# Kernel optimization log

Hardware: AMD Instinct MI355X
Metric: run time of the kernel (lower is better)

The kernel has to match this reference:

```python
import jax, jax.numpy as jnp
import numpy as np

N_NODES = 100000
N_EDGES = 1600000
F_IN = 128
HID = 128  # nhid*2
NHID = 64
N_GRAPHS = 512
N_CLASSES = 10
NEG_SLOPE = 0.2  # PyG GATConv default


def setup_inputs() -> dict:
    key = jax.random.key(0)
    ks = jax.random.split(key, 16)
    x = jax.random.normal(ks[0], (N_NODES, F_IN), dtype=jnp.float32)
    edge_index = jax.random.randint(ks[1], (2, N_EDGES), 0, N_NODES, dtype=jnp.int64)
    batch = jnp.sort(jax.random.randint(ks[2], (N_NODES,), 0, N_GRAPHS, dtype=jnp.int64))
    def lin(k, fan_in, shape):
        bound = 1.0 / np.sqrt(fan_in)
        return jax.random.uniform(k, shape, jnp.float32, -bound, bound)
    return {
        "x": x, "edge_index": edge_index, "batch": batch,
        "W1": lin(ks[3], F_IN, (F_IN, HID)),
        "a_src1": lin(ks[4], HID, (HID,)),
        "a_dst1": lin(ks[5], HID, (HID,)),
        "b1": jnp.zeros((HID,), jnp.float32),
        "W2": lin(ks[6], HID, (HID, HID)),
        "a_src2": lin(ks[7], HID, (HID,)),
        "a_dst2": lin(ks[8], HID, (HID,)),
        "b2": jnp.zeros((HID,), jnp.float32),
        "W_fc1": lin(ks[9], HID, (HID, NHID)),
        "b_fc1": lin(ks[10], HID, (NHID,)),
        "W_fc2": lin(ks[11], NHID, (NHID, N_CLASSES)),
        "b_fc2": lin(ks[12], NHID, (N_CLASSES,)),
    }


def gat_conv(x, src, dst, W, a_src, a_dst, b):
    # h = W x ; attention e_ij = LeakyReLU(a_src.h_i + a_dst.h_j), softmax over
    # incoming edges of each destination j, then scatter-add aggregation.
    h = x @ W                                   # [N, H]
    alpha_s = h @ a_src                         # [N]
    alpha_d = h @ a_dst                         # [N]
    e = jax.nn.leaky_relu(alpha_s[src] + alpha_d[dst], NEG_SLOPE)  # [E]
    n = x.shape[0]
    m = jax.ops.segment_max(e, dst, num_segments=n)                # per-dst max
    ex = jnp.exp(e - m[dst])
    denom = jax.ops.segment_sum(ex, dst, num_segments=n)
    alpha = ex / denom[dst]                                        # [E]
    out = jax.ops.segment_sum(alpha[:, None] * h[src], dst, num_segments=n)
    return out + b


def reference(x, edge_index, batch, W1, a_src1, a_dst1, b1,
              W2, a_src2, a_dst2, b2, W_fc1, b_fc1, W_fc2, b_fc2):
    n = x.shape[0]
    # GATConv default add_self_loops=True
    loops = jnp.arange(n, dtype=edge_index.dtype)
    src = jnp.concatenate([edge_index[0], loops])
    dst = jnp.concatenate([edge_index[1], loops])

    h = jax.nn.selu(gat_conv(x, src, dst, W1, a_src1, a_dst1, b1))
    h = jax.nn.selu(gat_conv(h, src, dst, W2, a_src2, a_dst2, b2))

    # global mean pool over graphs
    sums = jax.ops.segment_sum(h, batch, num_segments=N_GRAPHS)
    cnts = jax.ops.segment_sum(jnp.ones((n,), h.dtype), batch, num_segments=N_GRAPHS)
    pooled = jax.nn.selu(sums / jnp.maximum(cnts, 1.0)[:, None])   # [G, H]

    g = jax.nn.selu(pooled @ W_fc1 + b_fc1)
    # dropout p=0.5 is identity in eval mode
    logits = g @ W_fc2 + b_fc2
    return jax.nn.log_softmax(logits, axis=-1)
```

## Files before the change

kernel.cpp:

```cpp
#include <hip/hip_runtime.h>
#include <hip/hip_bf16.h>

#define NEG_SLOPE 0.2f
typedef unsigned int uint32;

#define BSHIFT 9
#define BSIZE 512
#define MAXB 256
#define PCHUNK 4096
#define BSTRIDE 12288

typedef __attribute__((ext_vector_type(8))) __bf16 bf16x8;
typedef __attribute__((ext_vector_type(4))) float f32x4;

__device__ __forceinline__ float selu_f(float x) {
    const float a = 1.6732632423543772f, s = 1.0507009873554805f;
    return x > 0.0f ? s * x : s * a * (__expf(x) - 1.0f);
}

__device__ __forceinline__ unsigned short f2bf(float x) {
    uint32 u = __float_as_uint(x);
    uint32 r = (u + 0x7fff + ((u >> 16) & 1)) >> 16;
    return (unsigned short)r;
}
__device__ __forceinline__ float bf_lo(uint32 g) { return __uint_as_float(g << 16); }
__device__ __forceinline__ float bf_hi(uint32 g) { return __uint_as_float(g & 0xffff0000u); }

__global__ __launch_bounds__(256) void prep9(const float* __restrict__ W1,
                                             const float* __restrict__ W2,
                                             unsigned short* __restrict__ Wb,
                                             const int* __restrict__ batch,
                                             int* __restrict__ gstart,
                                             int N, int G) {
    int b = blockIdx.x, t = threadIdx.x;
    if (b < 2) {
        const float* W = b ? W2 : W1;
        unsigned short* oh = Wb + (size_t)b * 32768;
        unsigned short* ol = oh + 16384;
        for (int d = t; d < 16384; d += 256) {
            int j = d & 7, nn = (d >> 3) & 127, g = d >> 10;
            float v = W[(g * 8 + j) * 128 + nn];
            uint32 hu = f2bf(v);
            float hv = __uint_as_float(hu << 16);
            oh[d] = (unsigned short)hu;
            ol[d] = f2bf(v - hv);
        }
    } else {
        int i = (b - 2) * 256 + t;
        if (i < N) {
            int bb = batch[i];
            int bp = (i == 0) ? -1 : batch[i - 1];
            for (int q = bp + 1; q <= bb; ++q) gstart[q] = i;
            if (i == N - 1)
                for (int q = bb + 1; q <= G; ++q) gstart[q] = N;
        }
    }
}

__global__ __launch_bounds__(256) void partition_edges(const int* __restrict__ ei,
                                                       int* __restrict__ gcur0,
                                                       uint32* __restrict__ tmp,
                                                       int E, int TOT) {
    __shared__ int lcnt[MAXB];
    __shared__ int lstart[MAXB];
    __shared__ int lcur[MAXB];
    __shared__ int gbase[MAXB];
    __shared__ uint32 staged[PCHUNK];
    __shared__ unsigned char bslot[PCHUNK];
    int t = threadIdx.x;
    int eb = blockIdx.x * PCHUNK;
    int sreg[16], dreg[16];
    #pragma unroll
    for (int k = 0; k < 16; ++k) {
        int e = eb + k * 256 + t;
        if (e < TOT) {
            if (e < E) { sreg[k] = ei[e]; dreg[k] = ei[E + e]; }
            else       { sreg[k] = dreg[k] = e - E; }
        } else dreg[k] = -1;
    }
    lcnt[t] = 0;
    __syncthreads();
    #pragma unroll
    for (int k = 0; k < 16; ++k)
        if (dreg[k] >= 0) atomicAdd(&lcnt[dreg[k] >> BSHIFT], 1);
    __syncthreads();
    int v = lcnt[t];
    lstart[t] = v;
    __syncthreads();
    for (int off = 1; off < 256; off <<= 1) {
        int add = (t >= off) ? lstart[t - off] : 0;
        __syncthreads();
        lstart[t] += add;
        __syncthreads();
    }
    int ex = lstart[t] - v;
    __syncthreads();
    lstart[t] = ex;
    lcur[t] = ex;
    if (v > 0) gbase[t] = t * BSTRIDE + atomicAdd(&gcur0[t], v);
    __syncthreads();
    #pragma unroll
    for (int k = 0; k < 16; ++k) {
        int d = dreg[k];
        if (d >= 0) {
            int b = d >> BSHIFT;
            int p = atomicAdd(&lcur[b], 1);
            staged[p] = ((uint32)(d & (BSIZE - 1)) << 17) | (uint32)sreg[k];
            bslot[p] = (unsigned char)b;
        }
    }
    __syncthreads();
    int nvalid = TOT - eb; if (nvalid > PCHUNK) nvalid = PCHUNK;
    for (int i = t; i < nvalid; i += 256) {
        int b = bslot[i];
        tmp[gbase[b] + (i - lstart[b])] = staged[i];
    }
}

__global__ __launch_bounds__(256) void bucket_build(const uint32* __restrict__ tmp,
                                                    const int* __restrict__ gcur0,
                                                    int* __restrict__ rowptr,
                                                    int* __restrict__ rowend,
                                                    int* __restrict__ col,
                                                    int N, int NB) {
    __shared__ int cnt[BSIZE];
    __shared__ int sums[256];
    int b = blockIdx.x, t = threadIdx.x;
    int lo = b << BSHIFT;
    int nn = N - lo; if (nn > BSIZE) nn = BSIZE;
    cnt[t] = 0; cnt[t + 256] = 0;
    __syncthreads();
    int ebeg = b * BSTRIDE;
    int eend = ebeg + gcur0[b];
    for (int i = ebeg + t; i < eend; i += 256)
        atomicAdd(&cnt[tmp[i] >> 17], 1);
    __syncthreads();
    int c0 = cnt[2 * t], c1 = cnt[2 * t + 1];
    int s2 = c0 + c1;
    sums[t] = s2;
    __syncthreads();
    for (int off = 1; off < 256; off <<= 1) {
        int add = (t >= off) ? sums[t - off] : 0;
        __syncthreads();
        sums[t] += add;
        __syncthreads();
    }
    int ex = sums[t] - s2;
    int st0 = ebeg + ex, st1 = st0 + c0;
    if (2 * t < nn)     { rowptr[lo + 2 * t] = st0;     rowend[lo + 2 * t] = st0 + c0; }
    if (2 * t + 1 < nn) { rowptr[lo + 2 * t + 1] = st1; rowend[lo + 2 * t + 1] = st1 + c1; }
    cnt[2 * t] = st0; cnt[2 * t + 1] = st1;
    __syncthreads();
    for (int i = ebeg + t; i < eend; i += 256) {
        uint32 u = tmp[i];
        int p = atomicAdd(&cnt[u >> 17], 1);
        col[p] = (int)(u & 0x1FFFFu);
    }
}

__device__ __forceinline__ void gemm_core(const bf16x8 ah[2][4],
                                          const __bf16* Wl,
                                          const float* a_src, const float* a_dst,
                                          uint32* hb, float* as_, float* ad_,
                                          int rbase, int n, int col16, int quad) {
    f32x4 acc[2][8];
    #pragma unroll
    for (int mt = 0; mt < 2; ++mt)
        #pragma unroll
        for (int t = 0; t < 8; ++t) acc[mt][t] = (f32x4)(0.0f);

    #pragma unroll
    for (int c = 0; c < 4; ++c) {
        #pragma unroll
        for (int t = 0; t < 8; ++t) {
            int off = (((c * 4 + quad) * 128) + t * 16 + col16) * 8;
            bf16x8 bh = *(const bf16x8*)&Wl[off];
            bf16x8 bl = *(const bf16x8*)&Wl[16384 + off];
            #pragma unroll
            for (int mt = 0; mt < 2; ++mt) {
                acc[mt][t] = __builtin_amdgcn_mfma_f32_16x16x32_bf16(ah[mt][c], bh, acc[mt][t], 0, 0, 0);
                acc[mt][t] = __builtin_amdgcn_mfma_f32_16x16x32_bf16(ah[mt][c], bl, acc[mt][t], 0, 0, 0);
            }
        }
    }
    float asv[8], adv[8];
    #pragma unroll
    for (int t = 0; t < 8; ++t) { asv[t] = a_src[t * 16 + col16]; adv[t] = a_dst[t * 16 + col16]; }
    #pragma unroll
    for (int mt = 0; mt < 2; ++mt) {
        #pragma unroll
        for (int reg = 0; reg < 4; ++reg) {
            float s = 0.0f, d = 0.0f;
            #pragma unroll
            for (int t = 0; t < 8; ++t) {
                float v = acc[mt][t][reg];
                s += v * asv[t]; d += v * adv[t];
            }
            #pragma unroll
            for (int off = 1; off < 16; off <<= 1) {
                s += __shfl_xor(s, off);
                d += __shfl_xor(d, off);
            }
            int r = rbase + mt * 16 + quad * 4 + reg;
            if (col16 == 0 && r < n) { as_[r] = s; ad_[r] = d; }
        }
    }
    #pragma unroll
    for (int mt = 0; mt < 2; ++mt)
    #pragma unroll
    for (int t = 0; t < 8; ++t)
    #pragma unroll
    for (int reg = 0; reg < 4; ++reg) {
        float v = acc[mt][t][reg];
        float p = __shfl_xor(v, 1);
        int r = rbase + mt * 16 + quad * 4 + reg;
        if (!(col16 & 1) && r < n) {
            uint32 pk = (uint32)f2bf(v) | ((uint32)f2bf(p) << 16);
            hb[(size_t)r * 64 + t * 8 + (col16 >> 1)] = pk;
        }
    }
}

__global__ __launch_bounds__(256) void gemm_mfma_f32(const float* __restrict__ X,
                                                     const unsigned short* __restrict__ Wbh,
                                                     const float* __restrict__ a_src,
                                                     const float* __restrict__ a_dst,
                                                     uint32* __restrict__ hb,
                                                     float* __restrict__ as_,
                                                     float* __restrict__ ad_, int n) {
    __shared__ __bf16 Wl[32768];
    const int tid = threadIdx.x;
    {
        const uint4* sw = (const uint4*)Wbh;
        uint4* dw = (uint4*)Wl;
        for (int i = tid; i < 4096; i += 256) dw[i] = sw[i];
    }
    const int lane = tid & 63, wid = tid >> 6;
    const int col16 = lane & 15, quad = lane >> 4;
    const int rbase = blockIdx.x * 128 + wid * 32;
    bf16x8 ah[2][4];
    #pragma unroll
    for (int mt = 0; mt < 2; ++mt) {
        int r = rbase + mt * 16 + col16;
        bool ok = (r < n);
        const float* xp = X + (size_t)r * 128;
        #pragma unroll
        for (int c = 0; c < 4; ++c) {
            int k0 = c * 32 + quad * 8;
            float4 x0 = ok ? *(const float4*)(xp + k0)     : make_float4(0.f,0.f,0.f,0.f);
            float4 x1 = ok ? *(const float4*)(xp + k0 + 4) : make_float4(0.f,0.f,0.f,0.f);
            float xs[8] = {x0.x,x0.y,x0.z,x0.w,x1.x,x1.y,x1.z,x1.w};
            #pragma unroll
            for (int j = 0; j < 8; ++j) ah[mt][c][j] = (__bf16)xs[j];
        }
    }
    __syncthreads();
    gemm_core(ah, Wl, a_src, a_dst, hb, as_, ad_, rbase, n, col16, quad);
}

__global__ __launch_bounds__(256) void gemm_mfma_bf16(const __bf16* __restrict__ X,
                                                      const unsigned short* __restrict__ Wbh,
                                                      const float* __restrict__ a_src,
                                                      const float* __restrict__ a_dst,
                                                      uint32* __restrict__ hb,
                                                      float* __restrict__ as_,
                                                      float* __restrict__ ad_, int n) {
    __shared__ __bf16 Wl[32768];
    const int tid = threadIdx.x;
    {
        const uint4* sw = (const uint4*)Wbh;
        uint4* dw = (uint4*)Wl;
        for (int i = tid; i < 4096; i += 256) dw[i] = sw[i];
    }
    const int lane = tid & 63, wid = tid >> 6;
    const int col16 = lane & 15, quad = lane >> 4;
    const int rbase = blockIdx.x * 128 + wid * 32;
    bf16x8 ah[2][4];
    const bf16x8 zz = (bf16x8)((__bf16)0.0f);
    #pragma unroll
    for (int mt = 0; mt < 2; ++mt) {
        int r = rbase + mt * 16 + col16;
        bool ok = (r < n);
        const __bf16* xp = X + (size_t)r * 128;
        #pragma unroll
        for (int c = 0; c < 4; ++c)
            ah[mt][c] = ok ? *(const bf16x8*)(xp + c * 32 + quad * 8) : zz;
    }
    __syncthreads();
    gemm_core(ah, Wl, a_src, a_dst, hb, as_, ad_, rbase, n, col16, quad);
}

__global__ __launch_bounds__(256) void gat_csr3(const int* __restrict__ rowptr,
                                                const int* __restrict__ rowend,
                                                const int* __restrict__ col,
                                                const uint2* __restrict__ hb2,
                                                const float* __restrict__ as_,
                                                const float* __restrict__ ad_,
                                                const float* __restrict__ bias,
                                                uint2* __restrict__ outb, int n) {
    __shared__ float wsh[4][2][32];
    __shared__ int   ssh[4][2][32];
    const int wid = threadIdx.x >> 6;
    const int lane = threadIdx.x & 63;
    const int sub = lane >> 5, l = lane & 31;
    const int node = blockIdx.x * 8 + wid * 2 + sub;
    const bool valid = node < n;
    int beg = 0, end = 0;
    if (valid) { beg = rowptr[node]; end = rowend[node]; }
    float add = valid ? ad_[node] : 0.0f;
    int deg = end - beg;
    int mdeg = max(deg, __shfl_xor(deg, 32));
    float m = -INFINITY, s = 0.0f;
    float a0 = 0.f, a1 = 0.f, a2 = 0.f, a3 = 0.f;
    for (int cb = 0; cb < mdeg; cb += 32) {
        int j = beg + cb + l;
        bool eok = (j < end);
        int srcn = eok ? col[j] : 0;
        float v = eok ? (as_[srcn] + add) : -INFINITY;
        v = (v > 0.0f) ? v : NEG_SLOPE * v;
        float cm = v;
        #pragma unroll
        for (int off = 16; off > 0; off >>= 1) cm = fmaxf(cm, __shfl_xor(cm, off));
        float nm = fmaxf(m, cm);
        float w = eok ? __expf(v - nm) : 0.0f;
        float ws = w;
        #pragma unroll
        for (int off = 16; off > 0; off >>= 1) ws += __shfl_xor(ws, off);
        float scale = (m == -INFINITY) ? 0.0f : __expf(m - nm);
        s = s * scale + ws;
        a0 *= scale; a1 *= scale; a2 *= scale; a3 *= scale;
        wsh[wid][sub][l] = w;
        ssh[wid][sub][l] = srcn;
        int cnt = end - beg - cb;
        cnt = (cnt > 32) ? 32 : (cnt < 0 ? 0 : cnt);
        int t = 0;
        for (; t + 8 <= cnt; t += 8) {
            int sr[8]; float wr[8]; uint2 g[8];
            #pragma unroll
            for (int q = 0; q < 8; ++q) { sr[q] = ssh[wid][sub][t + q]; wr[q] = wsh[wid][sub][t + q]; }
            #pragma unroll
            for (int q = 0; q < 8; ++q) g[q] = hb2[(uint32)sr[q] * 32u + l];
            #pragma unroll
            for (int q = 0; q < 8; ++q) {
                a0 += wr[q] * bf_lo(g[q].x); a1 += wr[q] * bf_hi(g[q].x);
                a2 += wr[q] * bf_lo(g[q].y); a3 += wr[q] * bf_hi(g[q].y);
            }
        }
        for (; t < cnt; ++t) {
            int sn = ssh[wid][sub][t];
            float wt = wsh[wid][sub][t];
            uint2 g = hb2[(uint32)sn * 32u + l];
            a0 += wt * bf_lo(g.x); a1 += wt * bf_hi(g.x);
            a2 += wt * bf_lo(g.y); a3 += wt * bf_hi(g.y);
        }
        m = nm;
    }
    if (valid) {
        float inv = 1.0f / s;
        float4 bv = *(const float4*)&bias[l * 4];
        float r0 = selu_f(a0 * inv + bv.x);
        float r1 = selu_f(a1 * inv + bv.y);
        float r2 = selu_f(a2 * inv + bv.z);
        float r3 = selu_f(a3 * inv + bv.w);
        uint2 o;
        o.x = (uint32)f2bf(r0) | ((uint32)f2bf(r1) << 16);
        o.y = (uint32)f2bf(r2) | ((uint32)f2bf(r3) << 16);
        outb[(uint32)node * 32u + l] = o;
    }
}

__global__ __launch_bounds__(128) void pool_head(const uint32* __restrict__ act,
                                                 const int* __restrict__ gstart,
                                                 const float* __restrict__ Wfc1,
                                                 const float* __restrict__ bfc1,
                                                 const float* __restrict__ Wfc2,
                                                 const float* __restrict__ bfc2,
                                                 float* __restrict__ out) {
    __shared__ float part[128][2];
    __shared__ float p[128];
    __shared__ float q[64];
    __shared__ float l[10];
    __shared__ float red[2];
    int g = blockIdx.x, t = threadIdx.x;
    int lo = gstart[g], hi = gstart[g + 1];
    int half = t >> 6, u = t & 63;
    float acc0 = 0.f, acc1 = 0.f;
    for (int nd = lo + half; nd < hi; nd += 2) {
        uint32 gv = act[(uint32)nd * 64u + u];
        acc0 += bf_lo(gv); acc1 += bf_hi(gv);
    }
    part[t][0] = acc0; part[t][1] = acc1;
    __syncthreads();
    if (half == 0) {
        float c = fmaxf((float)(hi - lo), 1.0f);
        p[2 * u]     = selu_f((acc0 + part[t + 64][0]) / c);
        p[2 * u + 1] = selu_f((acc1 + part[t + 64][1]) / c);
    }
    __syncthreads();
    if (t < 64) {
        float a = bfc1[t];
        #pragma unroll 8
        for (int k = 0; k < 128; ++k) a += p[k] * Wfc1[k * 64 + t];
        q[t] = selu_f(a);
    }
    __syncthreads();
    if (t < 10) {
        float a = bfc2[t];
        #pragma unroll
        for (int k = 0; k < 64; ++k) a += q[k] * Wfc2[k * 10 + t];
        l[t] = a;
    }
    __syncthreads();
    if (t == 0) {
        float mx = l[0];
        for (int c = 1; c < 10; ++c) mx = fmaxf(mx, l[c]);
        float sum = 0.0f;
        for (int c = 0; c < 10; ++c) sum += __expf(l[c] - mx);
        red[0] = mx; red[1] = logf(sum);
    }
    __syncthreads();
    if (t < 10) out[g * 10 + t] = l[t] - red[0] - red[1];
}

extern "C" void kernel_launch(void* const* d_in, const int* in_sizes, int n_in,
                              void* d_out, int out_size, void* d_ws, size_t ws_size,
                              hipStream_t stream) {
    const float* x      = (const float*)d_in[0];
    const int*   ei     = (const int*)d_in[1];
    const int*   batch  = (const int*)d_in[2];
    const float* W1     = (const float*)d_in[3];
    const float* asrc1  = (const float*)d_in[4];
    const float* adst1  = (const float*)d_in[5];
    const float* b1     = (const float*)d_in[6];
    const float* W2     = (const float*)d_in[7];
    const float* asrc2  = (const float*)d_in[8];
    const float* adst2  = (const float*)d_in[9];
    const float* b2     = (const float*)d_in[10];
    const float* Wfc1   = (const float*)d_in[11];
    const float* bfc1   = (const float*)d_in[12];
    const float* Wfc2   = (const float*)d_in[13];
    const float* bfc2   = (const float*)d_in[14];
    float* out = (float*)d_out;

    const int N = in_sizes[0] / 128;
    const int E = in_sizes[1] / 2;
    const int G = out_size / 10;
    const int TOT = E + N;
    const int NB = ((N - 1) >> BSHIFT) + 1;
    const int GB = (N + 255) / 256;
    const int PH = (TOT + PCHUNK - 1) / PCHUNK;
    const int GemmG = (N + 127) / 128;

    uint32* hb    = (uint32*)d_ws;
    uint32* h2b   = hb + (size_t)N * 64;
    uint32* tmp   = h2b + (size_t)N * 64;
    int*    col   = (int*)(tmp + (size_t)NB * BSTRIDE);
    float* as_    = (float*)(col + (size_t)NB * BSTRIDE);
    float* ad_    = as_ + N;
    int*   gstart = (int*)(ad_ + N);
    int*   rowptr = gstart + (G + 2);
    int*   rowend = rowptr + (N + 2);
    int*   gcur0  = rowend + (N + 2);
    unsigned short* Wb = (unsigned short*)(((uintptr_t)(gcur0 + MAXB) + 255) & ~(uintptr_t)255);

    const int gatGrid = (N + 7) / 8;

    hipMemsetAsync(gcur0, 0, MAXB * 4, stream);
    prep9<<<2 + GB, 256, 0, stream>>>(W1, W2, Wb, batch, gstart, N, G);
    partition_edges<<<PH, 256, 0, stream>>>(ei, gcur0, tmp, E, TOT);
    bucket_build<<<NB, 256, 0, stream>>>(tmp, gcur0, rowptr, rowend, col, N, NB);

    gemm_mfma_f32<<<GemmG, 256, 0, stream>>>(x, Wb, asrc1, adst1, hb, as_, ad_, N);
    gat_csr3<<<gatGrid, 256, 0, stream>>>(rowptr, rowend, col, (const uint2*)hb, as_, ad_, b1, (uint2*)h2b, N);

    gemm_mfma_bf16<<<GemmG, 256, 0, stream>>>((const __bf16*)h2b, Wb + 32768, asrc2, adst2, hb, as_, ad_, N);
    gat_csr3<<<gatGrid, 256, 0, stream>>>(rowptr, rowend, col, (const uint2*)hb, as_, ad_, b2, (uint2*)h2b, N);

    pool_head<<<G, 128, 0, stream>>>(h2b, gstart, Wfc1, bfc1, Wfc2, bfc2, out);
}
```

Baseline: 401.7 us.

## Aggregate GAT with 16 lanes per node, wide loads, no running max

The CSR attention aggregation kernel now gives each destination node 16 lanes instead of 32, so each wave handles four nodes. Each lane loads a uint4 of eight bf16 features and accumulates with packed two-wide FMAs. The online-softmax running max and its rescaling are removed, so exp is taken on the raw logit. This cuts shuffles and rescale work, but it can overflow if attention logits are large. Separately, edge partitioning uses half-size chunks (8 edges per thread), and bucket_build runs with 1024 threads per block for its counting and scatter passes.

After: 399.4 us. No clear change (-0.6%).

```diff
diff --git a/kernel.cpp b/kernel.cpp
--- a/kernel.cpp
+++ b/kernel.cpp
@@ -7,11 +7,13 @@
 #define BSHIFT 9
 #define BSIZE 512
 #define MAXB 256
-#define PCHUNK 4096
+#define PCHUNK 2048
+#define PEPT 8
 #define BSTRIDE 12288
 
 typedef __attribute__((ext_vector_type(8))) __bf16 bf16x8;
 typedef __attribute__((ext_vector_type(4))) float f32x4;
+typedef __attribute__((ext_vector_type(2))) float f32x2;
 
 __device__ __forceinline__ float selu_f(float x) {
     const float a = 1.6732632423543772f, s = 1.0507009873554805f;
@@ -69,9 +71,9 @@
     __shared__ unsigned char bslot[PCHUNK];
     int t = threadIdx.x;
     int eb = blockIdx.x * PCHUNK;
-    int sreg[16], dreg[16];
-    #pragma unroll
-    for (int k = 0; k < 16; ++k) {
+    int sreg[PEPT], dreg[PEPT];
+    #pragma unroll
+    for (int k = 0; k < PEPT; ++k) {
         int e = eb + k * 256 + t;
         if (e < TOT) {
             if (e < E) { sreg[k] = ei[e]; dreg[k] = ei[E + e]; }
@@ -81,7 +83,7 @@
     lcnt[t] = 0;
     __syncthreads();
     #pragma unroll
-    for (int k = 0; k < 16; ++k)
+    for (int k = 0; k < PEPT; ++k)
         if (dreg[k] >= 0) atomicAdd(&lcnt[dreg[k] >> BSHIFT], 1);
     __syncthreads();
     int v = lcnt[t];
@@ -100,7 +102,7 @@
     if (v > 0) gbase[t] = t * BSTRIDE + atomicAdd(&gcur0[t], v);
     __syncthreads();
     #pragma unroll
-    for (int k = 0; k < 16; ++k) {
+    for (int k = 0; k < PEPT; ++k) {
         int d = dreg[k];
         if (d >= 0) {
             int b = d >> BSHIFT;
@@ -117,41 +119,46 @@
     }
 }
 
-__global__ __launch_bounds__(256) void bucket_build(const uint32* __restrict__ tmp,
-                                                    const int* __restrict__ gcur0,
-                                                    int* __restrict__ rowptr,
-                                                    int* __restrict__ rowend,
-                                                    int* __restrict__ col,
-                                                    int N, int NB) {
+__global__ __launch_bounds__(1024) void bucket_build(const uint32* __restrict__ tmp,
+                                                     const int* __restrict__ gcur0,
+                                                     int* __restrict__ rowptr,
+                                                     int* __restrict__ rowend,
+                                                     int* __restrict__ col,
+                                                     int N, int NB) {
     __shared__ int cnt[BSIZE];
     __shared__ int sums[256];
     int b = blockIdx.x, t = threadIdx.x;
     int lo = b << BSHIFT;
     int nn = N - lo; if (nn > BSIZE) nn = BSIZE;
-    cnt[t] = 0; cnt[t + 256] = 0;
+    if (t < BSIZE) cnt[t] = 0;
     __syncthreads();
     int ebeg = b * BSTRIDE;
     int eend = ebeg + gcur0[b];
-    for (int i = ebeg + t; i < eend; i += 256)
+    for (int i = ebeg + t; i < eend; i += 1024)
         atomicAdd(&cnt[tmp[i] >> 17], 1);
     __syncthreads();
-    int c0 = cnt[2 * t], c1 = cnt[2 * t + 1];
-    int s2 = c0 + c1;
-    sums[t] = s2;
+    int c0 = 0, c1 = 0, s2 = 0;
+    if (t < 256) {
+        c0 = cnt[2 * t]; c1 = cnt[2 * t + 1];
+        s2 = c0 + c1;
+        sums[t] = s2;
+    }
     __syncthreads();
     for (int off = 1; off < 256; off <<= 1) {
-        int add = (t >= off) ? sums[t - off] : 0;
+        int add = (t < 256 && t >= off) ? sums[t - off] : 0;
         __syncthreads();
-        sums[t] += add;
+        if (t < 256) sums[t] += add;
         __syncthreads();
     }
-    int ex = sums[t] - s2;
-    int st0 = ebeg + ex, st1 = st0 + c0;
-    if (2 * t < nn)     { rowptr[lo + 2 * t] = st0;     rowend[lo + 2 * t] = st0 + c0; }
-    if (2 * t + 1 < nn) { rowptr[lo + 2 * t + 1] = st1; rowend[lo + 2 * t + 1] = st1 + c1; }
-    cnt[2 * t] = st0; cnt[2 * t + 1] = st1;
-    __syncthreads();
-    for (int i = ebeg + t; i < eend; i += 256) {
+    if (t < 256) {
+        int ex = sums[t] - s2;
+        int st0 = ebeg + ex, st1 = st0 + c0;
+        if (2 * t < nn)     { rowptr[lo + 2 * t] = st0;     rowend[lo + 2 * t] = st0 + c0; }
+        if (2 * t + 1 < nn) { rowptr[lo + 2 * t + 1] = st1; rowend[lo + 2 * t + 1] = st1 + c1; }
+        cnt[2 * t] = st0; cnt[2 * t + 1] = st1;
+    }
+    __syncthreads();
+    for (int i = ebeg + t; i < eend; i += 1024) {
         uint32 u = tmp[i];
         int p = atomicAdd(&cnt[u >> 17], 1);
         col[p] = (int)(u & 0x1FFFFu);
@@ -290,82 +297,105 @@
     gemm_core(ah, Wl, a_src, a_dst, hb, as_, ad_, rbase, n, col16, quad);
 }
 
-__global__ __launch_bounds__(256) void gat_csr3(const int* __restrict__ rowptr,
+__global__ __launch_bounds__(256) void gat_csr4(const int* __restrict__ rowptr,
                                                 const int* __restrict__ rowend,
                                                 const int* __restrict__ col,
-                                                const uint2* __restrict__ hb2,
+                                                const uint4* __restrict__ hb4,
                                                 const float* __restrict__ as_,
                                                 const float* __restrict__ ad_,
                                                 const float* __restrict__ bias,
-                                                uint2* __restrict__ outb, int n) {
-    __shared__ float wsh[4][2][32];
-    __shared__ int   ssh[4][2][32];
+                                                uint4* __restrict__ outb, int n) {
+    __shared__ float wsh[4][4][32];
+    __shared__ int   ssh[4][4][32];
     const int wid = threadIdx.x >> 6;
     const int lane = threadIdx.x & 63;
-    const int sub = lane >> 5, l = lane & 31;
-    const int node = blockIdx.x * 8 + wid * 2 + sub;
+    const int q = lane >> 4, l = lane & 15;
+    const int node = blockIdx.x * 16 + wid * 4 + q;
     const bool valid = node < n;
     int beg = 0, end = 0;
     if (valid) { beg = rowptr[node]; end = rowend[node]; }
     float add = valid ? ad_[node] : 0.0f;
     int deg = end - beg;
-    int mdeg = max(deg, __shfl_xor(deg, 32));
-    float m = -INFINITY, s = 0.0f;
-    float a0 = 0.f, a1 = 0.f, a2 = 0.f, a3 = 0.f;
+    int m1 = max(deg, __shfl_xor(deg, 16));
+    int mdeg = max(m1, __shfl_xor(m1, 32));
+    float s = 0.0f;
+    f32x2 ac[4];
+    #pragma unroll
+    for (int p = 0; p < 4; ++p) ac[p] = (f32x2)(0.0f);
+
     for (int cb = 0; cb < mdeg; cb += 32) {
-        int j = beg + cb + l;
-        bool eok = (j < end);
-        int srcn = eok ? col[j] : 0;
-        float v = eok ? (as_[srcn] + add) : -INFINITY;
-        v = (v > 0.0f) ? v : NEG_SLOPE * v;
-        float cm = v;
-        #pragma unroll
-        for (int off = 16; off > 0; off >>= 1) cm = fmaxf(cm, __shfl_xor(cm, off));
-        float nm = fmaxf(m, cm);
-        float w = eok ? __expf(v - nm) : 0.0f;
-        float ws = w;
-        #pragma unroll
-        for (int off = 16; off > 0; off >>= 1) ws += __shfl_xor(ws, off);
-        float scale = (m == -INFINITY) ? 0.0f : __expf(m - nm);
-        s = s * scale + ws;
-        a0 *= scale; a1 *= scale; a2 *= scale; a3 *= scale;
-        wsh[wid][sub][l] = w;
-        ssh[wid][sub][l] = srcn;
+        int j0 = beg + cb + l, j1 = j0 + 16;
+        bool e0 = (j0 < end), e1 = (j1 < end);
+        int s0 = e0 ? col[j0] : 0;
+        int s1 = e1 ? col[j1] : 0;
+        float v0 = as_[s0] + add;
+        float v1 = as_[s1] + add;
+        v0 = (v0 > 0.0f) ? v0 : NEG_SLOPE * v0;
+        v1 = (v1 > 0.0f) ? v1 : NEG_SLOPE * v1;
+        float w0 = e0 ? __expf(v0) : 0.0f;
+        float w1 = e1 ? __expf(v1) : 0.0f;
+        float ws = w0 + w1;
+        #pragma unroll
+        for (int off = 8; off > 0; off >>= 1) ws += __shfl_xor(ws, off);
+        s += ws;
+        wsh[wid][q][l] = w0;       wsh[wid][q][l + 16] = w1;
+        ssh[wid][q][l] = s0;       ssh[wid][q][l + 16] = s1;
+
         int cnt = end - beg - cb;
         cnt = (cnt > 32) ? 32 : (cnt < 0 ? 0 : cnt);
         int t = 0;
-        for (; t + 8 <= cnt; t += 8) {
-            int sr[8]; float wr[8]; uint2 g[8];
-            #pragma unroll
-            for (int q = 0; q < 8; ++q) { sr[q] = ssh[wid][sub][t + q]; wr[q] = wsh[wid][sub][t + q]; }
-            #pragma unroll
-            for (int q = 0; q < 8; ++q) g[q] = hb2[(uint32)sr[q] * 32u + l];
-            #pragma unroll
-            for (int q = 0; q < 8; ++q) {
-                a0 += wr[q] * bf_lo(g[q].x); a1 += wr[q] * bf_hi(g[q].x);
-                a2 += wr[q] * bf_lo(g[q].y); a3 += wr[q] * bf_hi(g[q].y);
+        for (; t + 4 <= cnt; t += 4) {
+            int sr[4]; float wr[4]; uint4 g[4];
+            #pragma unroll
+            for (int k = 0; k < 4; ++k) { sr[k] = ssh[wid][q][t + k]; wr[k] = wsh[wid][q][t + k]; }
+            #pragma unroll
+            for (int k = 0; k < 4; ++k) g[k] = hb4[(uint32)sr[k] * 16u + l];
+            #pragma unroll
+            for (int k = 0; k < 4; ++k) {
+                f32x2 wv = (f32x2)wr[k];
+                f32x2 u0 = { bf_lo(g[k].x), bf_hi(g[k].x) };
+                f32x2 u1 = { bf_lo(g[k].y), bf_hi(g[k].y) };
+                f32x2 u2 = { bf_lo(g[k].z), bf_hi(g[k].z) };
+                f32x2 u3 = { bf_lo(g[k].w), bf_hi(g[k].w) };
+                ac[0] = __builtin_elementwise_fma(wv, u0, ac[0]);
+                ac[1] = __builtin_elementwise_fma(wv, u1, ac[1]);
+                ac[2] = __builtin_elementwise_fma(wv, u2, ac[2]);
+                ac[3] = __builtin_elementwise_fma(wv, u3, ac[3]);
             }
         }
         for (; t < cnt; ++t) {
-            int sn = ssh[wid][sub][t];
-            float wt = wsh[wid][sub][t];
-            uint2 g = hb2[(uint32)sn * 32u + l];
-            a0 += wt * bf_lo(g.x); a1 += wt * bf_hi(g.x);
-            a2 += wt * bf_lo(g.y); a3 += wt * bf_hi(g.y);
-        }
-        m = nm;
+            int sn = ssh[wid][q][t];
+            float wt = wsh[wid][q][t];
+            uint4 g = hb4[(uint32)sn * 16u + l];
+            f32x2 wv = (f32x2)wt;
+            f32x2 u0 = { bf_lo(g.x), bf_hi(g.x) };
+            f32x2 u1 = { bf_lo(g.y), bf_hi(g.y) };
+            f32x2 u2 = { bf_lo(g.z), bf_hi(g.z) };
+            f32x2 u3 = { bf_lo(g.w), bf_hi(g.w) };
+            ac[0] = __builtin_elementwise_fma(wv, u0, ac[0]);
+            ac[1] = __builtin_elementwise_fma(wv, u1, ac[1]);
+            ac[2] = __builtin_elementwise_fma(wv, u2, ac[2]);
+            ac[3] = __builtin_elementwise_fma(wv, u3, ac[3]);
+        }
     }
     if (valid) {
         float inv = 1.0f / s;
-        float4 bv = *(const float4*)&bias[l * 4];
-        float r0 = selu_f(a0 * inv + bv.x);
-        float r1 = selu_f(a1 * inv + bv.y);
-        float r2 = selu_f(a2 * inv + bv.z);
-        float r3 = selu_f(a3 * inv + bv.w);
-        uint2 o;
+        float4 b0 = *(const float4*)&bias[l * 8];
+        float4 b1 = *(const float4*)&bias[l * 8 + 4];
+        float r0 = selu_f(ac[0].x * inv + b0.x);
+        float r1 = selu_f(ac[0].y * inv + b0.y);
+        float r2 = selu_f(ac[1].x * inv + b0.z);
+        float r3 = selu_f(ac[1].y * inv + b0.w);
+        float r4 = selu_f(ac[2].x * inv + b1.x);
+        float r5 = selu_f(ac[2].y * inv + b1.y);
+        float r6 = selu_f(ac[3].x * inv + b1.z);
+        float r7 = selu_f(ac[3].y * inv + b1.w);
+        uint4 o;
         o.x = (uint32)f2bf(r0) | ((uint32)f2bf(r1) << 16);
         o.y = (uint32)f2bf(r2) | ((uint32)f2bf(r3) << 16);
-        outb[(uint32)node * 32u + l] = o;
+        o.z = (uint32)f2bf(r4) | ((uint32)f2bf(r5) << 16);
+        o.w = (uint32)f2bf(r6) | ((uint32)f2bf(r7) << 16);
+        outb[(uint32)node * 16u + l] = o;
     }
 }
 
@@ -463,18 +493,18 @@
     int*   gcur0  = rowend + (N + 2);
     unsigned short* Wb = (unsigned short*)(((uintptr_t)(gcur0 + MAXB) + 255) & ~(uintptr_t)255);
 
-    const int gatGrid = (N + 7) / 8;
+    const int gatGrid = (N + 15) / 16;
 
     hipMemsetAsync(gcur0, 0, MAXB * 4, stream);
     prep9<<<2 + GB, 256, 0, stream>>>(W1, W2, Wb, batch, gstart, N, G);
     partition_edges<<<PH, 256, 0, stream>>>(ei, gcur0, tmp, E, TOT);
-    bucket_build<<<NB, 256, 0, stream>>>(tmp, gcur0, rowptr, rowend, col, N, NB);
+    bucket_build<<<NB, 1024, 0, stream>>>(tmp, gcur0, rowptr, rowend, col, N, NB);
 
     gemm_mfma_f32<<<GemmG, 256, 0, stream>>>(x, Wb, asrc1, adst1, hb, as_, ad_, N);
-    gat_csr3<<<gatGrid, 256, 0, stream>>>(rowptr, rowend, col, (const uint2*)hb, as_, ad_, b1, (uint2*)h2b, N);
+    gat_csr4<<<gatGrid, 256, 0, stream>>>(rowptr, rowend, col, (const uint4*)hb, as_, ad_, b1, (uint4*)h2b, N);
 
     gemm_mfma_bf16<<<GemmG, 256, 0, stream>>>((const __bf16*)h2b, Wb + 32768, asrc2, adst2, hb, as_, ad_, N);
-    gat_csr3<<<gatGrid, 256, 0, stream>>>(rowptr, rowend, col, (const uint2*)hb, as_, ad_, b2, (uint2*)h2b, N);
+    gat_csr4<<<gatGrid, 256, 0, stream>>>(rowptr, rowend, col, (const uint2*)hb ? (const uint4*)hb : (const uint4*)hb, as_, ad_, b2, (uint4*)h2b, N);
 
     pool_head<<<G, 128, 0, stream>>>(h2b, gstart, Wfc1, bfc1, Wfc2, bfc2, out);
 }
```
